# Performance work log

Hardware: AMD Instinct MI355X
Metric: run time of the kernel (lower is better)

The kernel has to match this reference:

```python
import jax, jax.numpy as jnp
import numpy as np

DIM = 1024
NUM_HEADS = 16
NUM_KV_HEADS = 4
HEAD_DIM = DIM // NUM_HEADS
KV_DIM = NUM_KV_HEADS * HEAD_DIM
PARTIAL_ROPE_DIM = 32
ROPE_BASE = 10000.0
LORA_RANK = 4
NUM_LORA_STEPS = 2
LORA_SCALE = 1.0
B, S = 2, 2048


def _rms_norm(x):
    eps = jnp.asarray(jnp.finfo(x.dtype).eps, x.dtype)
    return x * jax.lax.rsqrt(jnp.mean(x * x, axis=-1, keepdims=True) + eps)


def _rope_cos_sin(seq_len, dtype):
    half = PARTIAL_ROPE_DIM // 2
    inv_freq = 1.0 / (ROPE_BASE ** (jnp.arange(0, PARTIAL_ROPE_DIM, 2, dtype=jnp.float32) / PARTIAL_ROPE_DIM))
    t = jnp.arange(seq_len, dtype=jnp.float32)
    freqs = jnp.outer(t, inv_freq)  # [S, half]
    return jnp.cos(freqs).astype(dtype), jnp.sin(freqs).astype(dtype)


def _apply_rope_partial(x, cos, sin):
    # x: [B, H, S, D]; rotate first PARTIAL_ROPE_DIM dims, pass the rest.
    half = PARTIAL_ROPE_DIM // 2
    x1 = x[..., :half]
    x2 = x[..., half:PARTIAL_ROPE_DIM]
    xp = x[..., PARTIAL_ROPE_DIM:]
    c = cos[None, None, :, :]
    s = sin[None, None, :, :]
    return jnp.concatenate([x1 * c + x2 * s, -x1 * s + x2 * c, xp], axis=-1)


def setup_inputs() -> dict:
    key = jax.random.key(0)
    ks = jax.random.split(key, 12)
    std = 0.02
    return {
        "x": jax.random.normal(ks[0], (B, S, DIM), jnp.float32),
        "Wq": jax.random.normal(ks[1], (DIM, DIM), jnp.float32) * std,
        "Wk": jax.random.normal(ks[2], (KV_DIM, DIM), jnp.float32) * std,
        "Wv": jax.random.normal(ks[3], (KV_DIM, DIM), jnp.float32) * std,
        "Wproj": jax.random.normal(ks[4], (DIM, DIM), jnp.float32) * std,
        "q_gain": jnp.full((NUM_HEADS,), 1.0, jnp.float32),
        "lora_A_q": jax.random.normal(ks[5], (NUM_LORA_STEPS, LORA_RANK, DIM), jnp.float32) * std,
        "lora_B_q": jax.random.normal(ks[6], (NUM_LORA_STEPS, DIM, LORA_RANK), jnp.float32) * std,
        "lora_A_v": jax.random.normal(ks[7], (NUM_LORA_STEPS, LORA_RANK, DIM), jnp.float32) * std,
        "lora_B_v": jax.random.normal(ks[8], (NUM_LORA_STEPS, KV_DIM, LORA_RANK), jnp.float32) * std,
        "step_idx": 0,
    }


def reference(x, Wq, Wk, Wv, Wproj, q_gain, lora_A_q, lora_B_q, lora_A_v, lora_B_v, step_idx):
    bsz, seqlen, dim = x.shape
    q = x @ Wq.T
    v = x @ Wv.T
    if 0 <= step_idx < NUM_LORA_STEPS:
        q = q + LORA_SCALE * ((x @ lora_A_q[step_idx].T) @ lora_B_q[step_idx].T)
        v = v + LORA_SCALE * ((x @ lora_A_v[step_idx].T) @ lora_B_v[step_idx].T)
    k = x @ Wk.T

    q = q.reshape(bsz, seqlen, NUM_HEADS, HEAD_DIM).transpose(0, 2, 1, 3)      # [B,H,S,D]
    k = k.reshape(bsz, seqlen, NUM_KV_HEADS, HEAD_DIM).transpose(0, 2, 1, 3)   # [B,Hkv,S,D]
    v = v.reshape(bsz, seqlen, NUM_KV_HEADS, HEAD_DIM).transpose(0, 2, 1, 3)

    q = _rms_norm(q)
    k = _rms_norm(k)

    cos, sin = _rope_cos_sin(seqlen, q.dtype)
    q = _apply_rope_partial(q, cos, sin)
    k = _apply_rope_partial(k, cos, sin)

    q = q * q_gain.astype(q.dtype)[None, :, None, None]

    # GQA causal SDPA
    groups = NUM_HEADS // NUM_KV_HEADS
    qg = q.reshape(bsz, NUM_KV_HEADS, groups, seqlen, HEAD_DIM)
    scale = 1.0 / np.sqrt(HEAD_DIM)
    scores = jnp.einsum('bkgsd,bktd->bkgst', qg, k) * scale  # [B,Hkv,G,S,S]
    causal = jnp.tril(jnp.ones((seqlen, seqlen), bool))
    scores = jnp.where(causal[None, None, None], scores, jnp.asarray(-jnp.inf, scores.dtype))
    attn = jax.nn.softmax(scores, axis=-1)
    y = jnp.einsum('bkgst,bktd->bkgsd', attn, v)
    y = y.reshape(bsz, NUM_HEADS, seqlen, HEAD_DIM).transpose(0, 2, 1, 3).reshape(bsz, seqlen, dim)
    return y @ Wproj.T
```

## Files before the change

### kernel.cpp

```cpp
#include <hip/hip_runtime.h>
#include <hip/hip_bf16.h>
#include <stdint.h>

#define DIM 1024
#define NH 16
#define NKV 4
#define HD 64
#define SEQ 2048
#define BATCH 2
#define RANK 4
#define NSTEPS 2

#define XN      4194304
#define WQ_END  5242880
#define WK_END  5505024
#define WV_END  5767168
#define CVT_BLOCKS 6656
#define LORA_BLOCKS 1024

typedef unsigned short u16;
typedef unsigned int u32;
typedef __attribute__((ext_vector_type(8))) __bf16 bf16x8;
typedef __attribute__((ext_vector_type(4))) float f32x4;

__device__ __forceinline__ float bf2f(u16 v) {
    u32 u = ((u32)v) << 16;
    return __builtin_bit_cast(float, u);
}
__device__ __forceinline__ u16 f2bf(float f) {
    u32 u = __builtin_bit_cast(u32, f);
    u32 r = (u + 0x7fffu + ((u >> 16) & 1u)) >> 16;
    return (u16)r;
}
__device__ __forceinline__ u32 pk2(float a, float b) {
    return (u32)f2bf(a) | ((u32)f2bf(b) << 16);
}
__device__ __forceinline__ void glds16(const u16* g, u16* l) {
    __builtin_amdgcn_global_load_lds(
        (const __attribute__((address_space(1))) u32*)g,
        (__attribute__((address_space(3))) u32*)l, 16, 0, 0);
}

__global__ __launch_bounds__(256) void k_prep(
    const float* __restrict__ x, const float* __restrict__ Wq,
    const float* __restrict__ Wk, const float* __restrict__ Wv,
    const float* __restrict__ Wp, u16* __restrict__ dst,
    const float* __restrict__ Aq, const float* __restrict__ Av,
    const int* __restrict__ step_p, float* __restrict__ tq, float* __restrict__ tv)
{
    int bx = blockIdx.x;
    if (bx < CVT_BLOCKS) {
        int e = (bx * 256 + threadIdx.x) * 4;
        const float* src;
        if (e < XN)          src = x  + e;
        else if (e < WQ_END) src = Wq + (e - XN);
        else if (e < WK_END) src = Wk + (e - WQ_END);
        else if (e < WV_END) src = Wv + (e - WK_END);
        else                 src = Wp + (e - WV_END);
        float4 v = *(const float4*)src;
        *(uint2*)(dst + e) = make_uint2(pk2(v.x, v.y), pk2(v.z, v.w));
        return;
    }
    int wave = ((bx - CVT_BLOCKS) * 256 + threadIdx.x) >> 6;
    int lane = threadIdx.x & 63;
    int step = step_p[0];
    int valid = (step >= 0 && step < NSTEPS);
    int sc = valid ? step : 0;
    const float* xr = x + wave * DIM + lane * 16;
    float xf[16];
#pragma unroll
    for (int q = 0; q < 4; q++) {
        float4 v4 = *(const float4*)(xr + q * 4);
        xf[q * 4 + 0] = v4.x; xf[q * 4 + 1] = v4.y;
        xf[q * 4 + 2] = v4.z; xf[q * 4 + 3] = v4.w;
    }
    float sums[8];
#pragma unroll
    for (int j = 0; j < 8; j++) {
        const float* ar = (j < 4 ? Aq + sc * RANK * DIM + j * DIM
                                 : Av + sc * RANK * DIM + (j - 4) * DIM) + lane * 16;
        float s = 0.f;
#pragma unroll
        for (int q = 0; q < 4; q++) {
            float4 a4 = *(const float4*)(ar + q * 4);
            s += xf[q * 4 + 0] * a4.x + xf[q * 4 + 1] * a4.y
               + xf[q * 4 + 2] * a4.z + xf[q * 4 + 3] * a4.w;
        }
#pragma unroll
        for (int o = 32; o > 0; o >>= 1) s += __shfl_xor(s, o, 64);
        sums[j] = s;
    }
    if (!valid) {
#pragma unroll
        for (int j = 0; j < 8; j++) sums[j] = 0.f;
    }
    if (lane == 0) {
        tq[wave * 4 + 0] = sums[0]; tq[wave * 4 + 1] = sums[1];
        tq[wave * 4 + 2] = sums[2]; tq[wave * 4 + 3] = sums[3];
        tv[wave * 4 + 0] = sums[4]; tv[wave * 4 + 1] = sums[5];
        tv[wave * 4 + 2] = sums[6]; tv[wave * 4 + 3] = sums[7];
    }
}

template<bool CF32>
__global__ __launch_bounds__(256) void k_gemm(
    const u16* __restrict__ A, const u16* __restrict__ B,
    void* __restrict__ Cptr, int Ntiles, int N)
{
    __shared__ __align__(16) u16 As[8192];
    __shared__ __align__(16) u16 Bs[4096];
    int bx = blockIdx.x;
    int bn = bx % Ntiles, bm = bx / Ntiles;
    int t = threadIdx.x, lane = t & 63, w = t >> 6;
    int wy = w >> 1, wx = w & 1;
    int wb = t & ~63;
    f32x4 acc[4][2];
#pragma unroll
    for (int i = 0; i < 4; i++)
#pragma unroll
        for (int j = 0; j < 2; j++) acc[i][j] = (f32x4){0.f, 0.f, 0.f, 0.f};

    int goffA[4], goffB[2];
#pragma unroll
    for (int u = 0; u < 4; u++) {
        int idx = u * 256 + t;
        int grp = idx >> 6;
        int quad = (idx >> 4) & 3, m = idx & 15;
        goffA[u] = ((grp >> 1) * 16 + m) * DIM + (grp & 1) * 32 + quad * 8;
    }
#pragma unroll
    for (int u = 0; u < 2; u++) {
        int idx = u * 256 + t;
        int grp = idx >> 6;
        int quad = (idx >> 4) & 3, m = idx & 15;
        goffB[u] = ((grp >> 1) * 16 + m) * DIM + (grp & 1) * 32 + quad * 8;
    }
    const u16* Ab = A + bm * 128 * DIM;
    const u16* Bb = B + bn * 64 * DIM;

#pragma unroll 1
    for (int kb = 0; kb < 16; kb++) {
        int k0 = kb * 64;
        __syncthreads();
#pragma unroll
        for (int u = 0; u < 4; u++)
            glds16(Ab + goffA[u] + k0, As + (u * 256 + wb) * 8);
#pragma unroll
        for (int u = 0; u < 2; u++)
            glds16(Bb + goffB[u] + k0, Bs + (u * 256 + wb) * 8);
        __syncthreads();
#pragma unroll
        for (int c = 0; c < 2; c++) {
            bf16x8 af[4], bfr[2];
#pragma unroll
            for (int i = 0; i < 4; i++) {
                int mt = wy * 4 + i;
                af[i] = *(bf16x8*)(As + ((mt * 2 + c) * 64 + lane) * 8);
            }
#pragma unroll
            for (int j = 0; j < 2; j++) {
                int nt = wx * 2 + j;
                bfr[j] = *(bf16x8*)(Bs + ((nt * 2 + c) * 64 + lane) * 8);
            }
#pragma unroll
            for (int i = 0; i < 4; i++)
#pragma unroll
                for (int j = 0; j < 2; j++)
                    acc[i][j] = __builtin_amdgcn_mfma_f32_16x16x32_bf16(af[i], bfr[j], acc[i][j], 0, 0, 0);
        }
    }
    int quad = lane >> 4, n16 = lane & 15;
#pragma unroll
    for (int i = 0; i < 4; i++) {
#pragma unroll
        for (int j = 0; j < 2; j++) {
            int col = bn * 64 + wx * 32 + j * 16 + n16;
#pragma unroll
            for (int r = 0; r < 4; r++) {
                int rowm = bm * 128 + wy * 64 + i * 16 + quad * 4 + r;
                if (CF32) ((float*)Cptr)[rowm * N + col] = acc[i][j][r];
                else      ((u16*)Cptr)[rowm * N + col] = f2bf(acc[i][j][r]);
            }
        }
    }
}

#define NR_BLOCKS 20480
__global__ __launch_bounds__(256) void k_post(
    u16* __restrict__ qkv,
    const float* __restrict__ tq, const float* __restrict__ Bq,
    const float* __restrict__ gain,
    const float* __restrict__ tv, const float* __restrict__ Bv,
    const int* __restrict__ step_p, u16* __restrict__ vt)
{
    __shared__ __align__(16) u16 tile[64 * 64];
    int bx = blockIdx.x;
    int step = step_p[0];
    int valid = (step >= 0 && step < NSTEPS);
    int sc = valid ? step : 0;
    if (bx < NR_BLOCKS) {
        int wid = (bx * 256 + threadIdx.x) >> 6;
        int lane = threadIdx.x & 63;
        float val, postmul;
        u16* ptr;
        int s;
        if (wid < BATCH * NH * SEQ) {
            int b = wid >> 15;
            int h = (wid >> 11) & 15;
            s = wid & 2047;
            int row = b * SEQ + s;
            ptr = qkv + row * 1536 + h * HD + lane;
            val = bf2f(*ptr);
            const float* tr = tq + row * 4;
            float4 br = *(const float4*)(Bq + sc * DIM * RANK + (h * HD + lane) * RANK);
            val += tr[0] * br.x + tr[1] * br.y + tr[2] * br.z + tr[3] * br.w;
            postmul = gain[h] * 0.125f * 1.4426950408889634f;
        } else {
            int wk = wid - BATCH * NH * SEQ;
            int b = wk >> 13;
            int h = (wk >> 11) & 3;
            s = wk & 2047;
            int row = b * SEQ + s;
            ptr = qkv + row * 1536 + 1024 + h * HD + lane;
            val = bf2f(*ptr);
            postmul = 1.f;
        }
        float ss = val * val;
#pragma unroll
        for (int o = 32; o > 0; o >>= 1) ss += __shfl_xor(ss, o, 64);
        float rr = rsqrtf(ss * (1.f / 64.f) + 1.1920928955078125e-7f);
        float vn = val * rr;
        float partner = __shfl_xor(vn, 16, 64);
        float res;
        if (lane < 32) {
            int i = lane & 15;
            float invf = exp2f(-(float)i * 0.8304820237218405f);
            float ang = (float)s * invf;
            float cs = cosf(ang), sn = sinf(ang);
            res = (lane < 16) ? (vn * cs + partner * sn) : (-partner * sn + vn * cs);
        } else {
            res = vn;
        }
        *ptr = f2bf(res * postmul);
        return;
    }
    int vb = bx - NR_BLOCKS;
    int st = vb & 31, g = (vb >> 5) & 3, b = vb >> 7;
    int t = threadIdx.x;
    int s_l = t & 63, dq = t >> 6;
    int row = b * SEQ + st * 64 + s_l;
    const float* tr = tv + row * 4;
    float t0 = tr[0], t1 = tr[1], t2 = tr[2], t3 = tr[3];
    const u16* src = qkv + row * 1536 + 1280 + g * HD + dq * 16;
#pragma unroll
    for (int e = 0; e < 16; e++) {
        int d = dq * 16 + e;
        float4 br = *(const float4*)(Bv + sc * (NKV * HD) * RANK + (g * HD + d) * RANK);
        float v = bf2f(src[e]) + t0 * br.x + t1 * br.y + t2 * br.z + t3 * br.w;
        tile[d * 64 + s_l] = f2bf(v);
    }
    __syncthreads();
#pragma unroll
    for (int u = 0; u < 2; u++) {
        int chunk = u * 256 + t;
        int d = chunk >> 3, scn = chunk & 7;
        *(uint4*)(vt + ((b * NKV + g) * HD + d) * SEQ + st * 64 + scn * 8) =
            *(uint4*)(tile + d * 64 + scn * 8);
    }
}

__global__ __launch_bounds__(256) void k_attn(
    const u16* __restrict__ qkv, const u16* __restrict__ vt,
    const float* __restrict__ gain, u16* __restrict__ y,
    float* __restrict__ accP, float* __restrict__ psP)
{
    __shared__ __align__(16) u16 kf[4096];
    __shared__ __align__(16) u16 vf[4096];
    __shared__ __align__(16) u16 pb[4][1024];
    int bx = blockIdx.x;
    int pairsel = bx >> 1, role = bx & 1;
    int b = pairsel >> 8, h = (pairsel >> 4) & 15, qtsel = pairsel & 15;
    int g = h >> 2;
    int t = threadIdx.x, lane = t & 63, w = t >> 6, wb = t & ~63;
    int quad = lane >> 4, n16 = lane & 15;
    float negM = -11.67f * fabsf(gain[h]);

    const u16* kbase = qkv + b * SEQ * 1536 + 1024 + g * HD;
    const u16* vbase = vt + (b * NKV + g) * HD * SEQ;

    int koff0, koff1, voff0, voff1;
    {
        int s0 = t, r0 = s0 >> 3, c0 = (s0 & 7) ^ (r0 & 7);
        koff0 = r0 * 1536 + c0 * 8;  voff0 = r0 * 2048 + c0 * 8;
        int s1 = 256 + t, r1 = s1 >> 3, c1 = (s1 & 7) ^ (r1 & 7);
        koff1 = r1 * 1536 + c1 * 8;  voff1 = r1 * 2048 + c1 * 8;
    }
    int swb = n16 & 7;
    int o0 = n16 * 8 + (quad ^ swb);
    int o1 = n16 * 8 + ((4 + quad) ^ swb);
    u16* pw = pb[w];

    f32x4 acc[4];
    float ps;
    bf16x8 qlo, qhi;
    int qrow;

    auto reset_acc = [&]() {
#pragma unroll
        for (int i = 0; i < 4; i++) acc[i] = (f32x4){0.f, 0.f, 0.f, 0.f};
        ps = 0.f;
    };
    auto load_q = [&](int qt) {
        qrow = qt * 64 + w * 16 + n16;
        const u16* qp = qkv + (b * SEQ + qrow) * 1536 + h * HD + quad * 8;
        qlo = *(const bf16x8*)qp;
        qhi = *(const bf16x8*)(qp + 32);
    };
    auto tile = [&](int kt) {
        __syncthreads();
        const u16* kp = kbase + kt * (64 * 1536);
        const u16* vp = vbase + kt * 64;
        glds16(kp + koff0, kf + wb * 8);
        glds16(kp + koff1, kf + (256 + wb) * 8);
        glds16(vp + voff0, vf + wb * 8);
        glds16(vp + voff1, vf + (256 + wb) * 8);
        __syncthreads();
        f32x4 st[4];
#pragma unroll
        for (int nt = 0; nt < 4; nt++) {
            f32x4 sa = (f32x4){0.f, 0.f, 0.f, 0.f};
            sa = __builtin_amdgcn_mfma_f32_16x16x32_bf16(*(bf16x8*)(kf + (nt * 128 + o0) * 8), qlo, sa, 0, 0, 0);
            sa = __builtin_amdgcn_mfma_f32_16x16x32_bf16(*(bf16x8*)(kf + (nt * 128 + o1) * 8), qhi, sa, 0, 0, 0);
            st[nt] = sa;
        }
        float p[4][4];
        int kb0 = kt * 64;
#pragma unroll
        for (int nt = 0; nt < 4; nt++)
#pragma unroll
            for (int r = 0; r < 4; r++) {
                int key = kb0 + nt * 16 + quad * 4 + r;
                float e = exp2f(st[nt][r] + negM);
                e = (key > qrow) ? 0.f : e;
                p[nt][r] = e;
                ps += e;
            }
#pragma unroll
        for (int nt = 0; nt < 4; nt++) {
            u32 lo = pk2(p[nt][0], p[nt][1]);
            u32 hi = pk2(p[nt][2], p[nt][3]);
            int ck = nt >> 1;
            int qbk = (nt & 1) * 2 + (quad >> 1);
            int byteoff = (ck * 64 + qbk * 16 + n16) * 16 + (quad & 1) * 8;
            *(uint2*)((char*)pw + byteoff) = make_uint2(lo, hi);
        }
        asm volatile("s_waitcnt lgkmcnt(0)" ::: "memory");
#pragma unroll
        for (int ck = 0; ck < 2; ck++) {
            bf16x8 pfr = *(bf16x8*)(pw + (ck * 64 + lane) * 8);
            int oo = ck ? o1 : o0;
#pragma unroll
            for (int dt = 0; dt < 4; dt++)
                acc[dt] = __builtin_amdgcn_mfma_f32_16x16x32_bf16(*(bf16x8*)(vf + (dt * 128 + oo) * 8), pfr, acc[dt], 0, 0, 0);
        }
        asm volatile("" ::: "memory");
    };
    auto write_partial = [&](int pidx) {
        float pt = ps + __shfl_xor(ps, 16, 64);
        pt += __shfl_xor(pt, 32, 64);
        if (quad == 0) psP[pidx * 64 + w * 16 + n16] = pt;
        float* ap = accP + pidx * 4096 + w * 1024;
#pragma unroll
        for (int dt = 0; dt < 4; dt++)
#pragma unroll
            for (int r = 0; r < 4; r++)
                ap[dt * 256 + quad * 64 + r * 16 + n16] = acc[dt][r];
    };

    if (role == 0) {
        load_q(qtsel);
        reset_acc();
#pragma unroll 1
        for (int kt = 0; kt <= qtsel; kt++) tile(kt);
        {
            float pt = ps + __shfl_xor(ps, 16, 64);
            pt += __shfl_xor(pt, 32, 64);
            float li = 1.f / pt;
#pragma unroll
            for (int dt = 0; dt < 4; dt++) {
                uint2 o = make_uint2(pk2(acc[dt][0] * li, acc[dt][1] * li),
                                     pk2(acc[dt][2] * li, acc[dt][3] * li));
                int d = dt * 16 + quad * 4;
                *(uint2*)(y + (b * SEQ + qrow) * DIM + h * HD + d) = o;
            }
        }
        load_q(31 - qtsel);
        reset_acc();
#pragma unroll 1
        for (int kt = 0; kt <= 15 - qtsel; kt++) tile(kt);
        write_partial(pairsel * 2);
    } else {
        load_q(31 - qtsel);
        reset_acc();
#pragma unroll 1
        for (int kt = 16 - qtsel; kt <= 31 - qtsel; kt++) tile(kt);
        write_partial(pairsel * 2 + 1);
    }
}

__global__ __launch_bounds__(256) void k_comb(
    const float* __restrict__ accP, const float* __restrict__ psP,
    u16* __restrict__ y)
{
    int pairsel = blockIdx.x;
    int b = pairsel >> 8, h = (pairsel >> 4) & 15, qtsel = pairsel & 15;
    int qt = 31 - qtsel;
    int t = threadIdx.x, w = t >> 6, d = t & 63;
    const float* a0 = accP + (pairsel * 2) * 4096 + t * 16;
    const float* a1 = a0 + 4096;
    const float* p0 = psP + pairsel * 128 + w * 16;
    const float* p1 = p0 + 64;
    u16* yp = y + (b * SEQ + qt * 64 + w * 16) * DIM + h * HD + d;
#pragma unroll
    for (int i = 0; i < 4; i++) {
        float4 v0 = *(const float4*)(a0 + i * 4);
        float4 v1 = *(const float4*)(a1 + i * 4);
        float4 s0 = *(const float4*)(p0 + i * 4);
        float4 s1 = *(const float4*)(p1 + i * 4);
        yp[(i * 4 + 0) * DIM] = f2bf((v0.x + v1.x) / (s0.x + s1.x));
        yp[(i * 4 + 1) * DIM] = f2bf((v0.y + v1.y) / (s0.y + s1.y));
        yp[(i * 4 + 2) * DIM] = f2bf((v0.z + v1.z) / (s0.z + s1.z));
        yp[(i * 4 + 3) * DIM] = f2bf((v0.w + v1.w) / (s0.w + s1.w));
    }
}

extern "C" void kernel_launch(void* const* d_in, const int* in_sizes, int n_in,
                              void* d_out, int out_size, void* d_ws, size_t ws_size,
                              hipStream_t stream)
{
    (void)in_sizes; (void)n_in; (void)out_size; (void)ws_size;
    const float* x     = (const float*)d_in[0];
    const float* Wq    = (const float*)d_in[1];
    const float* Wk    = (const float*)d_in[2];
    const float* Wv    = (const float*)d_in[3];
    const float* Wproj = (const float*)d_in[4];
    const float* qgain = (const float*)d_in[5];
    const float* Aq    = (const float*)d_in[6];
    const float* Bq    = (const float*)d_in[7];
    const float* Av    = (const float*)d_in[8];
    const float* Bv    = (const float*)d_in[9];
    const int*   step  = (const int*)d_in[10];

    char* ws = (char*)d_ws;
    u16* wsbf = (u16*)ws;
    u16* xb   = wsbf;
    u16* wf   = wsbf + XN;
    u16* wp   = wsbf + WV_END;
    u16* qkv  = (u16*)(ws + 13631488);
    float* tq = (float*)(ws + 26214400);
    float* tv = tq + 16384;
    float* psP = (float*)(ws + 26345472);
    float* accP = (float*)d_out;
    u16* y    = xb;
    u16* vt   = wf;

    k_prep<<<CVT_BLOCKS + LORA_BLOCKS, 256, 0, stream>>>(x, Wq, Wk, Wv, Wproj, wsbf,
                                                         Aq, Av, step, tq, tv);
    k_gemm<false><<<768, 256, 0, stream>>>(xb, wf, qkv, 24, 1536);
    k_post<<<NR_BLOCKS + 256, 256, 0, stream>>>(qkv, tq, Bq, qgain, tv, Bv, step, vt);
    k_attn<<<1024, 256, 0, stream>>>(qkv, vt, qgain, y, accP, psP);
    k_comb<<<512, 256, 0, stream>>>(accP, psP, y);
    k_gemm<true><<<512, 256, 0, stream>>>(y, wp, d_out, 16, DIM);
}
```

Before: 233.8 us.

## Fuse LoRA, RMSNorm, RoPE and V transpose into QKV GEMM epilogue

Removes the separate k_post pass by applying the LoRA update, per-head RMS norm, partial RoPE, gain scaling and the V transpose directly in the QKV GEMM epilogue. The norm is reduced across the two wave columns through shared memory. Both GEMMs and the attention grid get block-index swizzles for better cache locality. The attention kernel skips causal masking on off-diagonal tiles and packs probabilities to bf16 by truncation with a byte permute instead of rounding. This saves a kernel launch and a full read/write of qkv, at the cost of a heavier epilogue and slightly different bf16 rounding of P.

```diff
diff --git a/kernel.cpp b/kernel.cpp
--- a/kernel.cpp
+++ b/kernel.cpp
@@ -34,6 +34,10 @@
 }
 __device__ __forceinline__ u32 pk2(float a, float b) {
     return (u32)f2bf(a) | ((u32)f2bf(b) << 16);
+}
+__device__ __forceinline__ u32 pk2t(float a, float b) {
+    return __builtin_amdgcn_perm(__builtin_bit_cast(u32, b),
+                                 __builtin_bit_cast(u32, a), 0x07060302u);
 }
 __device__ __forceinline__ void glds16(const u16* g, u16* l) {
     __builtin_amdgcn_global_load_lds(
@@ -102,15 +106,171 @@
     }
 }
 
-template<bool CF32>
-__global__ __launch_bounds__(256) void k_gemm(
+__global__ __launch_bounds__(256) void k_gemm_qkv(
     const u16* __restrict__ A, const u16* __restrict__ B,
-    void* __restrict__ Cptr, int Ntiles, int N)
+    u16* __restrict__ qkv, u16* __restrict__ vtb,
+    const float* __restrict__ tq, const float* __restrict__ Bq,
+    const float* __restrict__ tv, const float* __restrict__ Bv,
+    const float* __restrict__ gain, const int* __restrict__ step_p)
+{
+    __shared__ __align__(16) u16 As[8192];
+    __shared__ __align__(16) u16 Bs[4096];
+    __shared__ float sred[2][2][64];
+    int bx = blockIdx.x;
+    int bn = (bx & 7) * 3 + ((bx >> 3) % 3);
+    int bm = (bx >> 3) / 3;
+    int t = threadIdx.x, lane = t & 63, w = t >> 6;
+    int wy = w >> 1, wx = w & 1;
+    int wb = t & ~63;
+    int quad = lane >> 4, n16 = lane & 15;
+    f32x4 acc[4][2];
+#pragma unroll
+    for (int i = 0; i < 4; i++)
+#pragma unroll
+        for (int j = 0; j < 2; j++) acc[i][j] = (f32x4){0.f, 0.f, 0.f, 0.f};
+
+    int goffA[4], goffB[2];
+#pragma unroll
+    for (int u = 0; u < 4; u++) {
+        int idx = u * 256 + t;
+        int grp = idx >> 6;
+        int q_ = (idx >> 4) & 3, m = idx & 15;
+        goffA[u] = ((grp >> 1) * 16 + m) * DIM + (grp & 1) * 32 + q_ * 8;
+    }
+#pragma unroll
+    for (int u = 0; u < 2; u++) {
+        int idx = u * 256 + t;
+        int grp = idx >> 6;
+        int q_ = (idx >> 4) & 3, m = idx & 15;
+        goffB[u] = ((grp >> 1) * 16 + m) * DIM + (grp & 1) * 32 + q_ * 8;
+    }
+    const u16* Ab = A + bm * 128 * DIM;
+    const u16* Bb = B + bn * 64 * DIM;
+
+#pragma unroll 1
+    for (int kb = 0; kb < 16; kb++) {
+        int k0 = kb * 64;
+        __syncthreads();
+#pragma unroll
+        for (int u = 0; u < 4; u++)
+            glds16(Ab + goffA[u] + k0, As + (u * 256 + wb) * 8);
+#pragma unroll
+        for (int u = 0; u < 2; u++)
+            glds16(Bb + goffB[u] + k0, Bs + (u * 256 + wb) * 8);
+        __syncthreads();
+#pragma unroll
+        for (int c = 0; c < 2; c++) {
+            bf16x8 af[4], bfr[2];
+#pragma unroll
+            for (int i = 0; i < 4; i++)
+                af[i] = *(bf16x8*)(As + (((wy * 4 + i) * 2 + c) * 64 + lane) * 8);
+#pragma unroll
+            for (int j = 0; j < 2; j++)
+                bfr[j] = *(bf16x8*)(Bs + (((wx * 2 + j) * 2 + c) * 64 + lane) * 8);
+#pragma unroll
+            for (int i = 0; i < 4; i++)
+#pragma unroll
+                for (int j = 0; j < 2; j++)
+                    acc[i][j] = __builtin_amdgcn_mfma_f32_16x16x32_bf16(af[i], bfr[j], acc[i][j], 0, 0, 0);
+        }
+    }
+
+    int step = step_p[0];
+    int sc = (step >= 0 && step < NSTEPS) ? step : 0;
+    int col_l0 = wx * 32 + n16;
+    int row_base = bm * 128 + wy * 64 + quad * 4;
+
+    if (bn < 20) {
+        bool isq = (bn < 16);
+        if (isq) {
+            float4 B40 = *(const float4*)(Bq + (sc * DIM + bn * 64 + col_l0) * RANK);
+            float4 B41 = *(const float4*)(Bq + (sc * DIM + bn * 64 + col_l0 + 16) * RANK);
+#pragma unroll
+            for (int i = 0; i < 4; i++)
+#pragma unroll
+                for (int r = 0; r < 4; r++) {
+                    float4 t4 = *(const float4*)(tq + (row_base + i * 16 + r) * 4);
+                    acc[i][0][r] += t4.x * B40.x + t4.y * B40.y + t4.z * B40.z + t4.w * B40.w;
+                    acc[i][1][r] += t4.x * B41.x + t4.y * B41.y + t4.z * B41.z + t4.w * B41.w;
+                }
+        }
+        float sq[4][4];
+#pragma unroll
+        for (int i = 0; i < 4; i++)
+#pragma unroll
+            for (int r = 0; r < 4; r++) {
+                float s = acc[i][0][r] * acc[i][0][r] + acc[i][1][r] * acc[i][1][r];
+#pragma unroll
+                for (int o = 1; o < 16; o <<= 1) s += __shfl_xor(s, o, 64);
+                sq[i][r] = s;
+            }
+        if (n16 == 0) {
+#pragma unroll
+            for (int i = 0; i < 4; i++)
+#pragma unroll
+                for (int r = 0; r < 4; r++)
+                    sred[wy][wx][i * 16 + quad * 4 + r] = sq[i][r];
+        }
+        __syncthreads();
+        float postmul = isq ? (gain[bn] * 0.125f * 1.4426950408889634f) : 1.f;
+        int colbase = isq ? (bn * 64) : (1024 + (bn - 16) * 64);
+        float invf = exp2f(-(float)n16 * 0.8304820237218405f);
+#pragma unroll
+        for (int i = 0; i < 4; i++)
+#pragma unroll
+            for (int r = 0; r < 4; r++) {
+                int rl = i * 16 + quad * 4 + r;
+                float total = sq[i][r] + sred[wy][wx ^ 1][rl];
+                float rr = rsqrtf(total * (1.f / 64.f) + 1.1920928955078125e-7f);
+                int row = bm * 128 + wy * 64 + rl;
+                float v0 = acc[i][0][r] * rr, v1 = acc[i][1][r] * rr;
+                float o0, o1;
+                if (wx == 0) {
+                    float ang = (float)(row & 2047) * invf;
+                    float cs = cosf(ang), sn = sinf(ang);
+                    o0 = v0 * cs + v1 * sn;
+                    o1 = -v0 * sn + v1 * cs;
+                } else {
+                    o0 = v0; o1 = v1;
+                }
+                u16* dst = qkv + row * 1536 + colbase + col_l0;
+                dst[0]  = f2bf(o0 * postmul);
+                dst[16] = f2bf(o1 * postmul);
+            }
+    } else {
+        int g = bn - 20;
+        float4 B40 = *(const float4*)(Bv + (sc * (NKV * HD) + g * 64 + col_l0) * RANK);
+        float4 B41 = *(const float4*)(Bv + (sc * (NKV * HD) + g * 64 + col_l0 + 16) * RANK);
+#pragma unroll
+        for (int i = 0; i < 4; i++) {
+#pragma unroll
+            for (int r = 0; r < 4; r++) {
+                float4 t4 = *(const float4*)(tv + (row_base + i * 16 + r) * 4);
+                acc[i][0][r] += t4.x * B40.x + t4.y * B40.y + t4.z * B40.z + t4.w * B40.w;
+                acc[i][1][r] += t4.x * B41.x + t4.y * B41.y + t4.z * B41.z + t4.w * B41.w;
+            }
+            int row0 = row_base + i * 16;
+            int b = row0 >> 11, s0 = row0 & 2047;
+#pragma unroll
+            for (int j = 0; j < 2; j++) {
+                int d = col_l0 + j * 16;
+                uint2 pkv = make_uint2(pk2(acc[i][j][0], acc[i][j][1]),
+                                       pk2(acc[i][j][2], acc[i][j][3]));
+                *(uint2*)(vtb + ((b * NKV + g) * HD + d) * SEQ + s0) = pkv;
+            }
+        }
+    }
+}
+
+__global__ __launch_bounds__(256) void k_gemm_proj(
+    const u16* __restrict__ A, const u16* __restrict__ B,
+    float* __restrict__ C)
 {
     __shared__ __align__(16) u16 As[8192];
     __shared__ __align__(16) u16 Bs[4096];
     int bx = blockIdx.x;
-    int bn = bx % Ntiles, bm = bx / Ntiles;
+    int bn = (bx & 7) * 2 + ((bx >> 3) & 1);
+    int bm = bx >> 4;
     int t = threadIdx.x, lane = t & 63, w = t >> 6;
     int wy = w >> 1, wx = w & 1;
     int wb = t & ~63;
@@ -125,15 +285,15 @@
     for (int u = 0; u < 4; u++) {
         int idx = u * 256 + t;
         int grp = idx >> 6;
-        int quad = (idx >> 4) & 3, m = idx & 15;
-        goffA[u] = ((grp >> 1) * 16 + m) * DIM + (grp & 1) * 32 + quad * 8;
+        int q_ = (idx >> 4) & 3, m = idx & 15;
+        goffA[u] = ((grp >> 1) * 16 + m) * DIM + (grp & 1) * 32 + q_ * 8;
     }
 #pragma unroll
     for (int u = 0; u < 2; u++) {
         int idx = u * 256 + t;
         int grp = idx >> 6;
-        int quad = (idx >> 4) & 3, m = idx & 15;
-        goffB[u] = ((grp >> 1) * 16 + m) * DIM + (grp & 1) * 32 + quad * 8;
+        int q_ = (idx >> 4) & 3, m = idx & 15;
+        goffB[u] = ((grp >> 1) * 16 + m) * DIM + (grp & 1) * 32 + q_ * 8;
     }
     const u16* Ab = A + bm * 128 * DIM;
     const u16* Bb = B + bn * 64 * DIM;
@@ -153,15 +313,11 @@
         for (int c = 0; c < 2; c++) {
             bf16x8 af[4], bfr[2];
 #pragma unroll
-            for (int i = 0; i < 4; i++) {
-                int mt = wy * 4 + i;
-                af[i] = *(bf16x8*)(As + ((mt * 2 + c) * 64 + lane) * 8);
-            }
-#pragma unroll
-            for (int j = 0; j < 2; j++) {
-                int nt = wx * 2 + j;
-                bfr[j] = *(bf16x8*)(Bs + ((nt * 2 + c) * 64 + lane) * 8);
-            }
+            for (int i = 0; i < 4; i++)
+                af[i] = *(bf16x8*)(As + (((wy * 4 + i) * 2 + c) * 64 + lane) * 8);
+#pragma unroll
+            for (int j = 0; j < 2; j++)
+                bfr[j] = *(bf16x8*)(Bs + (((wx * 2 + j) * 2 + c) * 64 + lane) * 8);
 #pragma unroll
             for (int i = 0; i < 4; i++)
 #pragma unroll
@@ -171,102 +327,16 @@
     }
     int quad = lane >> 4, n16 = lane & 15;
 #pragma unroll
-    for (int i = 0; i < 4; i++) {
+    for (int i = 0; i < 4; i++)
 #pragma unroll
         for (int j = 0; j < 2; j++) {
             int col = bn * 64 + wx * 32 + j * 16 + n16;
 #pragma unroll
             for (int r = 0; r < 4; r++) {
                 int rowm = bm * 128 + wy * 64 + i * 16 + quad * 4 + r;
-                if (CF32) ((float*)Cptr)[rowm * N + col] = acc[i][j][r];
-                else      ((u16*)Cptr)[rowm * N + col] = f2bf(acc[i][j][r]);
+                C[rowm * DIM + col] = acc[i][j][r];
             }
         }
-    }
-}
-
-#define NR_BLOCKS 20480
-__global__ __launch_bounds__(256) void k_post(
-    u16* __restrict__ qkv,
-    const float* __restrict__ tq, const float* __restrict__ Bq,
-    const float* __restrict__ gain,
-    const float* __restrict__ tv, const float* __restrict__ Bv,
-    const int* __restrict__ step_p, u16* __restrict__ vt)
-{
-    __shared__ __align__(16) u16 tile[64 * 64];
-    int bx = blockIdx.x;
-    int step = step_p[0];
-    int valid = (step >= 0 && step < NSTEPS);
-    int sc = valid ? step : 0;
-    if (bx < NR_BLOCKS) {
-        int wid = (bx * 256 + threadIdx.x) >> 6;
-        int lane = threadIdx.x & 63;
-        float val, postmul;
-        u16* ptr;
-        int s;
-        if (wid < BATCH * NH * SEQ) {
-            int b = wid >> 15;
-            int h = (wid >> 11) & 15;
-            s = wid & 2047;
-            int row = b * SEQ + s;
-            ptr = qkv + row * 1536 + h * HD + lane;
-            val = bf2f(*ptr);
-            const float* tr = tq + row * 4;
-            float4 br = *(const float4*)(Bq + sc * DIM * RANK + (h * HD + lane) * RANK);
-            val += tr[0] * br.x + tr[1] * br.y + tr[2] * br.z + tr[3] * br.w;
-            postmul = gain[h] * 0.125f * 1.4426950408889634f;
-        } else {
-            int wk = wid - BATCH * NH * SEQ;
-            int b = wk >> 13;
-            int h = (wk >> 11) & 3;
-            s = wk & 2047;
-            int row = b * SEQ + s;
-            ptr = qkv + row * 1536 + 1024 + h * HD + lane;
-            val = bf2f(*ptr);
-            postmul = 1.f;
-        }
-        float ss = val * val;
-#pragma unroll
-        for (int o = 32; o > 0; o >>= 1) ss += __shfl_xor(ss, o, 64);
-        float rr = rsqrtf(ss * (1.f / 64.f) + 1.1920928955078125e-7f);
-        float vn = val * rr;
-        float partner = __shfl_xor(vn, 16, 64);
-        float res;
-        if (lane < 32) {
-            int i = lane & 15;
-            float invf = exp2f(-(float)i * 0.8304820237218405f);
-            float ang = (float)s * invf;
-            float cs = cosf(ang), sn = sinf(ang);
-            res = (lane < 16) ? (vn * cs + partner * sn) : (-partner * sn + vn * cs);
-        } else {
-            res = vn;
-        }
-        *ptr = f2bf(res * postmul);
-        return;
-    }
-    int vb = bx - NR_BLOCKS;
-    int st = vb & 31, g = (vb >> 5) & 3, b = vb >> 7;
-    int t = threadIdx.x;
-    int s_l = t & 63, dq = t >> 6;
-    int row = b * SEQ + st * 64 + s_l;
-    const float* tr = tv + row * 4;
-    float t0 = tr[0], t1 = tr[1], t2 = tr[2], t3 = tr[3];
-    const u16* src = qkv + row * 1536 + 1280 + g * HD + dq * 16;
-#pragma unroll
-    for (int e = 0; e < 16; e++) {
-        int d = dq * 16 + e;
-        float4 br = *(const float4*)(Bv + sc * (NKV * HD) * RANK + (g * HD + d) * RANK);
-        float v = bf2f(src[e]) + t0 * br.x + t1 * br.y + t2 * br.z + t3 * br.w;
-        tile[d * 64 + s_l] = f2bf(v);
-    }
-    __syncthreads();
-#pragma unroll
-    for (int u = 0; u < 2; u++) {
-        int chunk = u * 256 + t;
-        int d = chunk >> 3, scn = chunk & 7;
-        *(uint4*)(vt + ((b * NKV + g) * HD + d) * SEQ + st * 64 + scn * 8) =
-            *(uint4*)(tile + d * 64 + scn * 8);
-    }
 }
 
 __global__ __launch_bounds__(256) void k_attn(
@@ -278,9 +348,12 @@
     __shared__ __align__(16) u16 vf[4096];
     __shared__ __align__(16) u16 pb[4][1024];
     int bx = blockIdx.x;
-    int pairsel = bx >> 1, role = bx & 1;
-    int b = pairsel >> 8, h = (pairsel >> 4) & 15, qtsel = pairsel & 15;
-    int g = h >> 2;
+    int bgid = bx & 7, inner = bx >> 3;
+    int b = bgid >> 2, g = bgid & 3;
+    int h = g * 4 + (inner & 3);
+    int qtsel = (inner >> 2) & 15;
+    int role = (inner >> 6) & 1;
+    int pairsel = (b * 16 + h) * 16 + qtsel;
     int t = threadIdx.x, lane = t & 63, w = t >> 6, wb = t & ~63;
     int quad = lane >> 4, n16 = lane & 15;
     float negM = -11.67f * fabsf(gain[h]);
@@ -316,7 +389,7 @@
         qlo = *(const bf16x8*)qp;
         qhi = *(const bf16x8*)(qp + 32);
     };
-    auto tile = [&](int kt) {
+    auto tile = [&](int kt, bool diag) {
         __syncthreads();
         const u16* kp = kbase + kt * (64 * 1536);
         const u16* vp = vbase + kt * 64;
@@ -334,21 +407,32 @@
             st[nt] = sa;
         }
         float p[4][4];
-        int kb0 = kt * 64;
-#pragma unroll
-        for (int nt = 0; nt < 4; nt++)
-#pragma unroll
-            for (int r = 0; r < 4; r++) {
-                int key = kb0 + nt * 16 + quad * 4 + r;
-                float e = exp2f(st[nt][r] + negM);
-                e = (key > qrow) ? 0.f : e;
-                p[nt][r] = e;
-                ps += e;
-            }
+        if (diag) {
+            int kb0 = kt * 64;
+#pragma unroll
+            for (int nt = 0; nt < 4; nt++)
+#pragma unroll
+                for (int r = 0; r < 4; r++) {
+                    int key = kb0 + nt * 16 + quad * 4 + r;
+                    float e = exp2f(st[nt][r] + negM);
+                    e = (key > qrow) ? 0.f : e;
+                    p[nt][r] = e;
+                    ps += e;
+                }
+        } else {
+#pragma unroll
+            for (int nt = 0; nt < 4; nt++)
+#pragma unroll
+                for (int r = 0; r < 4; r++) {
+                    float e = exp2f(st[nt][r] + negM);
+                    p[nt][r] = e;
+                    ps += e;
+                }
+        }
 #pragma unroll
         for (int nt = 0; nt < 4; nt++) {
-            u32 lo = pk2(p[nt][0], p[nt][1]);
-            u32 hi = pk2(p[nt][2], p[nt][3]);
+            u32 lo = pk2t(p[nt][0], p[nt][1]);
+            u32 hi = pk2t(p[nt][2], p[nt][3]);
             int ck = nt >> 1;
             int qbk = (nt & 1) * 2 + (quad >> 1);
             int byteoff = (ck * 64 + qbk * 16 + n16) * 16 + (quad & 1) * 8;
@@ -381,7 +465,8 @@
         load_q(qtsel);
         reset_acc();
 #pragma unroll 1
-        for (int kt = 0; kt <= qtsel; kt++) tile(kt);
+        for (int kt = 0; kt < qtsel; kt++) tile(kt, false);
+        tile(qtsel, true);
         {
             float pt = ps + __shfl_xor(ps, 16, 64);
             pt += __shfl_xor(pt, 32, 64);
@@ -397,13 +482,14 @@
         load_q(31 - qtsel);
         reset_acc();
 #pragma unroll 1
-        for (int kt = 0; kt <= 15 - qtsel; kt++) tile(kt);
+        for (int kt = 0; kt <= 15 - qtsel; kt++) tile(kt, false);
         write_partial(pairsel * 2);
     } else {
         load_q(31 - qtsel);
         reset_acc();
 #pragma unroll 1
-        for (int kt = 16 - qtsel; kt <= 31 - qtsel; kt++) tile(kt);
+        for (int kt = 16 - qtsel; kt < 31 - qtsel; kt++) tile(kt, false);
+        tile(31 - qtsel, true);
         write_partial(pairsel * 2 + 1);
     }
 }
@@ -460,15 +546,14 @@
     float* tq = (float*)(ws + 26214400);
     float* tv = tq + 16384;
     float* psP = (float*)(ws + 26345472);
+    u16* vt   = (u16*)(ws + 26607616);
     float* accP = (float*)d_out;
     u16* y    = xb;
-    u16* vt   = wf;
 
     k_prep<<<CVT_BLOCKS + LORA_BLOCKS, 256, 0, stream>>>(x, Wq, Wk, Wv, Wproj, wsbf,
                                                          Aq, Av, step, tq, tv);
-    k_gemm<false><<<768, 256, 0, stream>>>(xb, wf, qkv, 24, 1536);
-    k_post<<<NR_BLOCKS + 256, 256, 0, stream>>>(qkv, tq, Bq, qgain, tv, Bv, step, vt);
+    k_gemm_qkv<<<768, 256, 0, stream>>>(xb, wf, qkv, vt, tq, Bq, tv, Bv, qgain, step);
     k_attn<<<1024, 256, 0, stream>>>(qkv, vt, qgain, y, accP, psP);
     k_comb<<<512, 256, 0, stream>>>(accP, psP, y);
-    k_gemm<true><<<512, 256, 0, stream>>>(y, wp, d_out, 16, DIM);
-}
+    k_gemm_proj<<<512, 256, 0, stream>>>(y, wp, (float*)d_out);
+}
```

Measured after the change: 216.9 us. 1.08x faster.
